# Performance work log

Hardware: AMD Instinct MI355X
Metric: run time of the kernel (lower is better)

## Reference

```python
import jax, jax.numpy as jnp
import numpy as np

N_MODELS = 90
L = 89  # each expert sees the 89 off-diagonal entries of its row
SLOPE = 0.33


def _leaky(v):
    return jnp.where(v >= 0, v, SLOPE * v)


def _basenet(x, W1, b1, W2, b2, W3, b3, Wfc, bfc):
    # x: [B, 1, 89, 1]  (NCHW); convs use kernel (3,1), stride 2, padding 1 on both dims,
    # exactly matching torch Conv2d(k=(3,1), padding=1, stride=2).
    def conv(v, W, b):
        o = jax.lax.conv_general_dilated(
            v, W, window_strides=(2, 2), padding=((1, 1), (1, 1)),
            dimension_numbers=("NCHW", "OIHW", "NCHW"))
        return _leaky(o + b[None, :, None, None])

    o = conv(x, W1, b1)   # [B,16,45,2]
    o = conv(o, W2, b2)   # [B,32,23,2]
    o = conv(o, W3, b3)   # [B,64,12,2]
    o = o.mean(axis=(2, 3))            # global avg pool -> [B,64]
    return _leaky(o @ Wfc.T + bfc)     # [B,1]


def setup_inputs() -> dict:
    key = jax.random.key(0)
    ks = jax.random.split(key, 9)
    B = 2048
    x = jax.random.normal(ks[0], (B, 1, 90, 90), dtype=jnp.float32)

    def p(k, shape, fan_in):
        bound = 1.0 / np.sqrt(fan_in)
        return jax.random.uniform(k, shape, jnp.float32, -bound, bound)

    # Stacked parameters for the 90 independent BaseNets (leading axis = expert).
    W1 = p(ks[1], (N_MODELS, 16, 1, 3, 1), 1 * 3 * 1)
    b1 = p(ks[2], (N_MODELS, 16), 1 * 3 * 1)
    W2 = p(ks[3], (N_MODELS, 32, 16, 3, 1), 16 * 3 * 1)
    b2 = p(ks[4], (N_MODELS, 32), 16 * 3 * 1)
    W3 = p(ks[5], (N_MODELS, 64, 32, 3, 1), 32 * 3 * 1)
    b3 = p(ks[6], (N_MODELS, 64), 32 * 3 * 1)
    Wfc = p(ks[7], (N_MODELS, 1, 64), 64)
    bfc = p(ks[8], (N_MODELS, 1), 64)
    return {"x": x, "W1": W1, "b1": b1, "W2": W2, "b2": b2,
            "W3": W3, "b3": b3, "Wfc": Wfc, "bfc": bfc}


def reference(x, W1, b1, W2, b2, W3, b3, Wfc, bfc):
    B = x.shape[0]
    # Expert i gathers row i of the 90x90 map, excluding the diagonal element (89 cols).
    idx = np.stack([np.concatenate([np.arange(i), np.arange(i + 1, N_MODELS)])
                    for i in range(N_MODELS)])  # [90, 89] static
    rows = jnp.arange(N_MODELS)[:, None]
    X = x[:, 0][:, rows, jnp.asarray(idx)]        # [B, 90, 89]
    X = X.transpose(1, 0, 2)[:, :, None, :, None]  # [90, B, 1, 89, 1]

    f = jax.vmap(_basenet, in_axes=(0,) * 9)
    outs = f(X, W1, b1, W2, b2, W3, b3, Wfc, bfc)  # [90, B, 1]
    return outs[:, :, 0].T                          # [B, 90]
```

## Files before the change

kernel.cpp:

```cpp
#include <hip/hip_runtime.h>


#define SLOPE 0.33f
#define NCHUNK 8
#define BATCH 2048

__device__ __forceinline__ float leaky(float v) {
    return v >= 0.0f ? v : SLOPE * v;
}

__global__ void __launch_bounds__(64) fused_expert_broadcast(
    const float* __restrict__ b1,
    const float* __restrict__ W2,
    const float* __restrict__ b2,
    const float* __restrict__ W3,
    const float* __restrict__ b3,
    const float* __restrict__ Wfc,
    const float* __restrict__ bfc,
    float* __restrict__ out)
{
    const int e     = blockIdx.x / NCHUNK;
    const int chunk = blockIdx.x % NCHUNK;
    const int t = threadIdx.x;

    __shared__ float a1s[16];
    __shared__ float t2s[32], m2s[32], u2s[32];

    if (t < 16) a1s[t] = leaky(b1[e * 16 + t]);
    __syncthreads();

    if (t < 32) {
        const float* w2 = W2 + (size_t)(e * 32 + t) * 16 * 3;
        float stop = 0.f, smid = 0.f, sbot = 0.f;
        #pragma unroll
        for (int c = 0; c < 16; ++c) {
            float w0 = w2[c * 3 + 0];
            float w1 = w2[c * 3 + 1];
            float w2v = w2[c * 3 + 2];
            float a = a1s[c];
            stop += a * (w1 + w2v);
            smid += a * (w0 + w1 + w2v);
            sbot += a * (w0 + w1);
        }
        float b = b2[e * 32 + t];
        t2s[t] = leaky(b + stop);
        m2s[t] = leaky(b + smid);
        u2s[t] = leaky(b + sbot);
    }
    __syncthreads();

    const float* w3 = W3 + (size_t)(e * 64 + t) * 32 * 3;
    float stop = 0.f, smid = 0.f, sbot = 0.f;
    #pragma unroll
    for (int c = 0; c < 32; ++c) {
        float w0 = w3[c * 3 + 0];
        float w1 = w3[c * 3 + 1];
        float w2v = w3[c * 3 + 2];
        float m = m2s[c];
        stop += w1 * t2s[c] + w2v * m;
        smid += (w0 + w1 + w2v) * m;
        sbot += w0 * m + w1 * u2s[c];
    }
    float b = b3[e * 64 + t];
    float pooled = (12.0f * leaky(b)
                    + leaky(b + stop)
                    + 10.0f * leaky(b + smid)
                    + leaky(b + sbot)) * (1.0f / 24.0f);

    float sum = Wfc[e * 64 + t] * pooled;
    #pragma unroll
    for (int off = 32; off > 0; off >>= 1)
        sum += __shfl_xor(sum, off, 64);
    const float val = leaky(sum + bfc[e]);

    const int rows_per_chunk = BATCH / NCHUNK;
    const int r0 = chunk * rows_per_chunk;
    #pragma unroll
    for (int i = 0; i < rows_per_chunk / 64; ++i) {
        int r = r0 + i * 64 + t;
        out[(size_t)r * 90 + e] = val;
    }
}

extern "C" void kernel_launch(void* const* d_in, const int* in_sizes, int n_in,
                              void* d_out, int out_size, void* d_ws, size_t ws_size,
                              hipStream_t stream) {
    const float* b1  = (const float*)d_in[2];
    const float* W2  = (const float*)d_in[3];
    const float* b2  = (const float*)d_in[4];
    const float* W3  = (const float*)d_in[5];
    const float* b3  = (const float*)d_in[6];
    const float* Wfc = (const float*)d_in[7];
    const float* bfc = (const float*)d_in[8];

    float* out = (float*)d_out;

    fused_expert_broadcast<<<90 * NCHUNK, 64, 0, stream>>>(
        b1, W2, b2, W3, b3, Wfc, bfc, out);
}
```

Before: 10.22 us.

## Pair experts per block, preload W3 rows into registers, write float2 outputs

```diff
diff --git a/kernel.cpp b/kernel.cpp
--- a/kernel.cpp
+++ b/kernel.cpp
@@ -9,7 +9,7 @@
     return v >= 0.0f ? v : SLOPE * v;
 }
 
-__global__ void __launch_bounds__(64) fused_expert_broadcast(
+__global__ void __launch_bounds__(128) fused_pair_broadcast(
     const float* __restrict__ b1,
     const float* __restrict__ W2,
     const float* __restrict__ b2,
@@ -19,66 +19,74 @@
     const float* __restrict__ bfc,
     float* __restrict__ out)
 {
-    const int e     = blockIdx.x / NCHUNK;
+    const int p     = blockIdx.x / NCHUNK;
     const int chunk = blockIdx.x % NCHUNK;
-    const int t = threadIdx.x;
+    const int w = threadIdx.x >> 6;
+    const int t = threadIdx.x & 63;
+    const int e = 2 * p + w;
 
-    __shared__ float a1s[16];
-    __shared__ float t2s[32], m2s[32], u2s[32];
+    __shared__ float t2s[2][32], m2s[2][32], u2s[2][32];
+    __shared__ float vals[2];
 
-    if (t < 16) a1s[t] = leaky(b1[e * 16 + t]);
-    __syncthreads();
+    const float* w3p = W3 + (size_t)(e * 64 + t) * 96;
+    float w3r[96];
+    #pragma unroll
+    for (int i = 0; i < 24; ++i)
+        *(float4*)&w3r[4 * i] = *(const float4*)&w3p[4 * i];
+    const float b3v  = b3[e * 64 + t];
+    const float wfcv = Wfc[e * 64 + t];
+    const float bfcv = bfc[e];
 
     if (t < 32) {
-        const float* w2 = W2 + (size_t)(e * 32 + t) * 16 * 3;
+        const float* w2 = W2 + (size_t)(e * 32 + t) * 48;
         float stop = 0.f, smid = 0.f, sbot = 0.f;
         #pragma unroll
         for (int c = 0; c < 16; ++c) {
-            float w0 = w2[c * 3 + 0];
-            float w1 = w2[c * 3 + 1];
+            float w0  = w2[c * 3 + 0];
+            float w1  = w2[c * 3 + 1];
             float w2v = w2[c * 3 + 2];
-            float a = a1s[c];
+            float a = leaky(b1[e * 16 + c]);
             stop += a * (w1 + w2v);
             smid += a * (w0 + w1 + w2v);
             sbot += a * (w0 + w1);
         }
         float b = b2[e * 32 + t];
-        t2s[t] = leaky(b + stop);
-        m2s[t] = leaky(b + smid);
-        u2s[t] = leaky(b + sbot);
+        t2s[w][t] = leaky(b + stop);
+        m2s[w][t] = leaky(b + smid);
+        u2s[w][t] = leaky(b + sbot);
     }
     __syncthreads();
 
-    const float* w3 = W3 + (size_t)(e * 64 + t) * 32 * 3;
     float stop = 0.f, smid = 0.f, sbot = 0.f;
     #pragma unroll
     for (int c = 0; c < 32; ++c) {
-        float w0 = w3[c * 3 + 0];
-        float w1 = w3[c * 3 + 1];
-        float w2v = w3[c * 3 + 2];
-        float m = m2s[c];
-        stop += w1 * t2s[c] + w2v * m;
+        float w0  = w3r[c * 3 + 0];
+        float w1  = w3r[c * 3 + 1];
+        float w2v = w3r[c * 3 + 2];
+        float m = m2s[w][c];
+        stop += w1 * t2s[w][c] + w2v * m;
         smid += (w0 + w1 + w2v) * m;
-        sbot += w0 * m + w1 * u2s[c];
+        sbot += w0 * m + w1 * u2s[w][c];
     }
-    float b = b3[e * 64 + t];
-    float pooled = (12.0f * leaky(b)
-                    + leaky(b + stop)
-                    + 10.0f * leaky(b + smid)
-                    + leaky(b + sbot)) * (1.0f / 24.0f);
+    float pooled = (12.0f * leaky(b3v)
+                    + leaky(b3v + stop)
+                    + 10.0f * leaky(b3v + smid)
+                    + leaky(b3v + sbot)) * (1.0f / 24.0f);
 
-    float sum = Wfc[e * 64 + t] * pooled;
+    float sum = wfcv * pooled;
     #pragma unroll
     for (int off = 32; off > 0; off >>= 1)
         sum += __shfl_xor(sum, off, 64);
-    const float val = leaky(sum + bfc[e]);
+    if (t == 0) vals[w] = leaky(sum + bfcv);
+    __syncthreads();
 
+    const float2 v2 = make_float2(vals[0], vals[1]);
     const int rows_per_chunk = BATCH / NCHUNK;
     const int r0 = chunk * rows_per_chunk;
     #pragma unroll
-    for (int i = 0; i < rows_per_chunk / 64; ++i) {
-        int r = r0 + i * 64 + t;
-        out[(size_t)r * 90 + e] = val;
+    for (int i = 0; i < rows_per_chunk / 128; ++i) {
+        int r = r0 + i * 128 + threadIdx.x;
+        *(float2*)&out[(size_t)r * 90 + 2 * p] = v2;
     }
 }
 
@@ -95,6 +103,6 @@
 
     float* out = (float*)d_out;
 
-    fused_expert_broadcast<<<90 * NCHUNK, 64, 0, stream>>>(
+    fused_pair_broadcast<<<45 * NCHUNK, 128, 0, stream>>>(
         b1, W2, b2, W3, b3, Wfc, bfc, out);
 }
```

New measurement: 11.94 us. +16.8%, slower.
